# Kernel tuning notes

Measured on AMD Instinct MI355X. Metric: run time of the kernel, lower is better.

## Reference

```python
import jax, jax.numpy as jnp
import numpy as np

B, T, IN, H, NCLS = 128, 512, 4, 256, 3


def _lstm_dir(x_tbi, w_ih, w_hh, b, reverse):
    """One direction of one LSTM layer. x_tbi: [T,B,in] -> ys [T,B,H].
    Gate order matches torch: i, f, g, o."""
    # Precompute input projections for all timesteps (one big GEMM).
    xp = jnp.einsum('tbi,gi->tbg', x_tbi, w_ih) + b  # [T,B,4H]
    nB = x_tbi.shape[1]
    nH = w_hh.shape[1]
    h0 = jnp.zeros((nB, nH), x_tbi.dtype)
    c0 = jnp.zeros((nB, nH), x_tbi.dtype)

    def step(carry, gx):
        h, c = carry
        g = gx + h @ w_hh.T  # [B,4H]
        i, f, gg, o = jnp.split(g, 4, axis=-1)
        c = jax.nn.sigmoid(f) * c + jax.nn.sigmoid(i) * jnp.tanh(gg)
        h = jax.nn.sigmoid(o) * jnp.tanh(c)
        return (h, c), h

    _, ys = jax.lax.scan(step, (h0, c0), xp, reverse=reverse)
    return ys  # [T,B,H], time-aligned with input for both directions


def _bilstm_layer(x_tbi, w_ih, w_hh, b):
    yf = _lstm_dir(x_tbi, w_ih[0], w_hh[0], b[0], reverse=False)
    yb = _lstm_dir(x_tbi, w_ih[1], w_hh[1], b[1], reverse=True)
    return jnp.concatenate([yf, yb], axis=-1)  # [T,B,2H]


def setup_inputs() -> dict:
    key = jax.random.key(0)
    ks = jax.random.split(key, 9)
    s = 0.05
    return {
        'x': jax.random.normal(ks[0], (B, T, IN), jnp.float32),
        'w_ih_l0': jax.random.normal(ks[1], (2, 4 * H, IN), jnp.float32) * s,
        'w_hh_l0': jax.random.normal(ks[2], (2, 4 * H, H), jnp.float32) * s,
        'b_l0': jax.random.normal(ks[3], (2, 4 * H), jnp.float32) * s,
        'w_ih_l1': jax.random.normal(ks[4], (2, 4 * H, 2 * H), jnp.float32) * s,
        'w_hh_l1': jax.random.normal(ks[5], (2, 4 * H, H), jnp.float32) * s,
        'b_l1': jax.random.normal(ks[6], (2, 4 * H), jnp.float32) * s,
        'w_out': jax.random.normal(ks[7], (NCLS, H), jnp.float32) * s,
        'b_out': jax.random.normal(ks[8], (NCLS,), jnp.float32) * s,
    }


def reference(x, w_ih_l0, w_hh_l0, b_l0, w_ih_l1, w_hh_l1, b_l1, w_out, b_out):
    xt = jnp.transpose(x, (1, 0, 2))  # [T,B,4] (time-major for scan)
    b0 = b_l0[:, None, :]  # broadcast over [T,B]
    b1 = b_l1[:, None, :]
    y0 = _bilstm_layer(xt, w_ih_l0, w_hh_l0, b0)   # [T,B,2H]
    y1 = _bilstm_layer(y0, w_ih_l1, w_hh_l1, b1)   # [T,B,2H]
    # sum directions, then take last timestep (torch: out[:,:,:H]+out[:,:,H:], out[:,-1,:])
    last = y1[-1, :, :H] + y1[-1, :, H:]           # [B,H]
    logits = last @ w_out.T + b_out                # [B,3]
    return jax.nn.softmax(logits, axis=1)
```

## Files before the change

### kernel.cpp

```cpp
#include <hip/hip_runtime.h>

typedef __attribute__((ext_vector_type(8))) short bf16x8;
typedef __attribute__((ext_vector_type(4))) float f32x4;
typedef __attribute__((ext_vector_type(4))) int   i32x4;

#define T_LEN 512
#define BATCH 128
#define HID   256
#define G4    1024
#define WPI8_STRIDE 262144

__device__ __forceinline__ float sigmf(float x){
  return __builtin_amdgcn_rcpf(1.0f + __expf(-x));
}
__device__ __forceinline__ float tanhf_(float x){
  return 1.0f - 2.0f*__builtin_amdgcn_rcpf(1.0f + __expf(2.0f*x));
}
__device__ __forceinline__ unsigned short f2bf(float f){
  union{float f;unsigned u;} v; v.f=f;
  unsigned r = v.u + 0x7FFF + ((v.u>>16)&1);
  return (unsigned short)(r>>16);
}
__device__ __forceinline__ float bf2f(unsigned short b){
  union{unsigned u;float f;} v; v.u = ((unsigned)b)<<16; return v.f;
}

__global__ void k_scales(const float* __restrict__ w_hh0, const float* __restrict__ w_hh1,
                         float* __restrict__ comb, float* __restrict__ s_inv){
  int idx = blockIdx.x*256 + threadIdx.x;
  if (idx >= 3*1024) return;
  int dl = idx >> 10, n = idx & 1023;
  const float* src = (dl < 2) ? (w_hh0 + ((size_t)dl*1024 + n)*256)
                              : (w_hh1 + (size_t)n*256);
  float m = 1e-20f;
  for (int k = 0; k < 256; k += 4){
    float4 v = *(const float4*)&src[k];
    m = fmaxf(m, fmaxf(fmaxf(fabsf(v.x), fabsf(v.y)), fmaxf(fabsf(v.z), fabsf(v.w))));
  }
  s_inv[idx] = 127.f / m;
  comb[idx]  = m / 16129.f;
}

__global__ void k_pack_i8(const float* __restrict__ w_hh0, const float* __restrict__ w_hh1,
                          const float* __restrict__ s_inv, char* __restrict__ wp){
  int idx = blockIdx.x*256 + threadIdx.x;
  if (idx >= 3*WPI8_STRIDE) return;
  int j    = idx & 15;
  int lane = (idx >> 4) & 63;
  int kk   = (idx >> 10) & 3;
  int tile = (idx >> 12) & 63;
  int dl   = idx >> 18;
  int g = tile & 3, s = tile >> 2;
  int n = g*256 + s*16 + (lane & 15);
  int k = kk*64 + ((lane >> 4) << 4) + j;
  const float* src = (dl < 2) ? (w_hh0 + ((size_t)dl*1024 + n)*256)
                              : (w_hh1 + (size_t)n*256);
  float v = src[k] * s_inv[dl*1024 + n];
  int q = (int)rintf(fminf(127.f, fmaxf(-127.f, v)));
  wp[idx] = (char)q;
}

__global__ void k_pack_wih1(const float* __restrict__ w, const float* __restrict__ b1,
                            unsigned short* __restrict__ o, float* __restrict__ b1perm){
  int idx = blockIdx.x*256 + threadIdx.x;
  if (idx >= 2*1024*512) return;
  int d     = idx >> 19;
  int rem   = idx & ((1 << 19) - 1);
  int n_out = rem >> 9;
  int k     = rem & 511;
  int n_src = d ? n_out
                : ((n_out & 3)*256 + (n_out >> 6)*16 + ((n_out >> 2) & 15));
  o[idx] = f2bf(w[((size_t)(d*1024 + n_src))*512 + k]);
  if (idx < 1024){
    int ns = (idx & 3)*256 + (idx >> 6)*16 + ((idx >> 2) & 15);
    b1perm[idx] = b1[ns];
  }
}

template<int MODE>
__global__ __launch_bounds__(512, 2) void k_rec4(
    const float* __restrict__ x,
    const char* __restrict__ wpack,
    const float* __restrict__ comb,
    const float* __restrict__ w_ih0,
    const float* __restrict__ b0,
    const unsigned short* __restrict__ xp,
    unsigned short* __restrict__ y0,
    float* __restrict__ hS)
{
  const int tid  = threadIdx.x;
  const int lane = tid & 63;
  const int w    = tid >> 6;
  int dir, bgrp, dl;
  if (MODE == 0){ dir = blockIdx.x >> 5; bgrp = blockIdx.x & 31; dl = dir; }
  else          { dir = 0; bgrp = blockIdx.x; dl = 2; }
  const int b0r = bgrp * 4;

  __shared__ __align__(16) char   A_lds[2][4*288];
  __shared__ __align__(16) float  x_lds[2][4][4];
  __shared__ __align__(16) float4 wv_lds[1024];
  __shared__ float bia_lds[1024];

  const i32x4* wpb = (const i32x4*)(wpack + (size_t)dl*WPI8_STRIDE);
  i32x4 breg[2][4][4];
  #pragma unroll
  for (int p = 0; p < 2; ++p)
    #pragma unroll
    for (int g = 0; g < 4; ++g)
      #pragma unroll
      for (int kk = 0; kk < 4; ++kk)
        breg[p][g][kk] = wpb[(((((2*w+p)*4 + g)*4) + kk) << 6) + lane];

  const int c   = lane & 15;
  const int bl  = lane >> 4;
  const int jc0 = (2*w)*16 + c;
  const int jc1 = jc0 + 16;

  float cmb_l[2][4];
  #pragma unroll
  for (int g = 0; g < 4; ++g){
    cmb_l[0][g] = comb[dl*1024 + g*256 + jc0];
    cmb_l[1][g] = comb[dl*1024 + g*256 + jc1];
  }

  for (int i = tid; i < 2*4*288; i += 512) ((char*)A_lds)[i] = 0;
  if (MODE == 0){
    for (int i = tid; i < 1024; i += 512){
      wv_lds[i]  = *(const float4*)&w_ih0[(size_t)(dir*1024 + i)*4];
      bia_lds[i] = b0[dir*1024 + i];
    }
    if (tid < 16){
      int row = tid >> 2, i = tid & 3;
      int t0 = dir ? (T_LEN-1) : 0;
      x_lds[0][row][i] = x[((size_t)(b0r+row)*T_LEN + t0)*4 + i];
    }
  }

  float c_reg[2] = {0.f, 0.f};

  uint2 cinC[2], cinN[2];
  if (MODE == 1){
    #pragma unroll
    for (int p = 0; p < 2; ++p)
      cinC[p] = *(const uint2*)&xp[((((size_t)0*32 + bgrp)*16 + (2*w+p))*64 + lane)*4];
  }

  for (int tt = 0; tt < T_LEN; ++tt){
    const int t = (MODE == 0 && dir) ? (T_LEN-1-tt) : tt;
    const char* Ac = A_lds[tt & 1];
    char* An = (char*)A_lds[(tt + 1) & 1];

    __syncthreads();

    i32x4 a[4];
    #pragma unroll
    for (int kk = 0; kk < 4; ++kk)
      a[kk] = *(const i32x4*)&Ac[(c >> 2)*288 + kk*64 + ((lane >> 4) << 4)];

    if (MODE == 1){
      int tn = (t + 1 < T_LEN) ? t + 1 : t;
      #pragma unroll
      for (int p = 0; p < 2; ++p)
        cinN[p] = *(const uint2*)&xp[((((size_t)tn*32 + bgrp)*16 + (2*w+p))*64 + lane)*4];
    }

    i32x4 acc[2][4];
    #pragma unroll
    for (int p = 0; p < 2; ++p)
      #pragma unroll
      for (int g = 0; g < 4; ++g){
        acc[p][g] = (i32x4){0,0,0,0};
        #pragma unroll
        for (int kk = 0; kk < 4; ++kk)
          acc[p][g] = __builtin_amdgcn_mfma_i32_16x16x64_i8(a[kk], breg[p][g][kk], acc[p][g], 0, 0, 0);
      }

    float4 xr;
    if (MODE == 0) xr = *(const float4*)&x_lds[tt & 1][bl][0];

    float hv[2];
    #pragma unroll
    for (int p = 0; p < 2; ++p){
      const int jc = p ? jc1 : jc0;
      float gv[4];
      if (MODE == 0){
        #pragma unroll
        for (int g = 0; g < 4; ++g){
          float4 wv4 = wv_lds[g*256 + jc];
          float t0 = fmaf(xr.x, wv4.x, bia_lds[g*256 + jc]);
          t0 = fmaf(xr.y, wv4.y, t0);
          t0 = fmaf(xr.z, wv4.z, t0);
          t0 = fmaf(xr.w, wv4.w, t0);
          gv[g] = fmaf((float)acc[p][g][0], cmb_l[p][g], t0);
        }
      } else {
        unsigned lo = cinC[p].x, hi = cinC[p].y;
        gv[0] = fmaf((float)acc[p][0][0], cmb_l[p][0], bf2f((unsigned short)(lo & 0xFFFF)));
        gv[1] = fmaf((float)acc[p][1][0], cmb_l[p][1], bf2f((unsigned short)(lo >> 16)));
        gv[2] = fmaf((float)acc[p][2][0], cmb_l[p][2], bf2f((unsigned short)(hi & 0xFFFF)));
        gv[3] = fmaf((float)acc[p][3][0], cmb_l[p][3], bf2f((unsigned short)(hi >> 16)));
      }
      float cc = sigmf(gv[1])*c_reg[p] + sigmf(gv[0])*tanhf_(gv[2]);
      c_reg[p] = cc;
      float h = sigmf(gv[3])*tanhf_(cc);
      hv[p] = h;
      float hcl = fminf(127.f, fmaxf(-127.f, h*127.f));
      An[bl*288 + jc] = (char)__float2int_rn(hcl);
      if (MODE == 1 && tt == T_LEN-1)
        hS[(size_t)(b0r + bl)*HID + jc] = h;
    }
    if (MODE == 0){
      unsigned pk;
      asm("v_cvt_pk_bf16_f32 %0, %1, %2" : "=v"(pk) : "v"(hv[0]), "v"(hv[1]));
      size_t yb = ((size_t)t*BATCH + (b0r + bl))*(2*HID) + dir*HID;
      y0[yb + jc0] = (unsigned short)(pk & 0xFFFFu);
      y0[yb + jc1] = (unsigned short)(pk >> 16);
    }

    if (MODE == 0 && tid < 16){
      int tn = dir ? (t > 0 ? t-1 : 0) : (t < T_LEN-1 ? t+1 : t);
      int row = tid >> 2, i = tid & 3;
      x_lds[(tt + 1) & 1][row][i] = x[((size_t)(b0r+row)*T_LEN + tn)*4 + i];
    }
    if (MODE == 1){ cinC[0] = cinN[0]; cinC[1] = cinN[1]; }
  }
}

template<int PLAIN>
__global__ __launch_bounds__(256) void k_gemm_bf(
    const unsigned short* __restrict__ A, const unsigned short* __restrict__ B,
    const float* __restrict__ bias, unsigned short* __restrict__ outF, float* __restrict__ outP)
{
  __shared__ __align__(16) unsigned short As[128*64];
  __shared__ __align__(16) unsigned short Bs[128*64];
  const int tid  = threadIdx.x;
  const int lane = tid & 63;
  const int w = tid >> 6, wm = w >> 1, wn = w & 1;
  const int t  = blockIdx.y;
  const int n0 = blockIdx.x * 128;

  f32x4 acc[4][4];
  #pragma unroll
  for (int i = 0; i < 4; ++i)
    #pragma unroll
    for (int jx = 0; jx < 4; ++jx) acc[i][jx] = (f32x4){0.f,0.f,0.f,0.f};

  const int sr = tid >> 3;
  const int sq = tid & 7;

  for (int k0 = 0; k0 < 512; k0 += 64){
    #pragma unroll
    for (int it = 0; it < 4; ++it){
      int r = sr + it*32;
      uint4 av = *(const uint4*)&A[((size_t)t*128 + r)*512 + k0 + sq*8];
      uint4 bv = *(const uint4*)&B[((size_t)(n0 + r))*512 + k0 + sq*8];
      *(uint4*)&As[r*64 + (sq ^ (r & 7))*8] = av;
      *(uint4*)&Bs[r*64 + (sq ^ (r & 7))*8] = bv;
    }
    __syncthreads();
    bf16x8 af[4][2], bfv[4][2];
    #pragma unroll
    for (int mt = 0; mt < 4; ++mt)
      #pragma unroll
      for (int kk = 0; kk < 2; ++kk){
        int row = wm*64 + mt*16 + (lane & 15);
        af[mt][kk] = *(const bf16x8*)&As[row*64 + ((kk*4 + (lane>>4)) ^ (row & 7))*8];
      }
    #pragma unroll
    for (int nl = 0; nl < 4; ++nl)
      #pragma unroll
      for (int kk = 0; kk < 2; ++kk){
        int row = wn*64 + nl*16 + (lane & 15);
        bfv[nl][kk] = *(const bf16x8*)&Bs[row*64 + ((kk*4 + (lane>>4)) ^ (row & 7))*8];
      }
    #pragma unroll
    for (int mt = 0; mt < 4; ++mt)
      #pragma unroll
      for (int nl = 0; nl < 4; ++nl){
        acc[mt][nl] = __builtin_amdgcn_mfma_f32_16x16x32_bf16(af[mt][0], bfv[nl][0], acc[mt][nl], 0,0,0);
        acc[mt][nl] = __builtin_amdgcn_mfma_f32_16x16x32_bf16(af[mt][1], bfv[nl][1], acc[mt][nl], 0,0,0);
      }
    __syncthreads();
  }

  #pragma unroll
  for (int mt = 0; mt < 4; ++mt){
    #pragma unroll
    for (int nl = 0; nl < 4; ++nl){
      int ng = n0 + wn*64 + nl*16 + (lane & 15);
      float bv = bias[ng];
      f32x4 v = acc[mt][nl];
      if (PLAIN){
        int mrow = wm*64 + mt*16 + (lane >> 4)*4;
        #pragma unroll
        for (int r = 0; r < 4; ++r)
          outP[((size_t)t*128 + mrow + r)*G4 + ng] = v[r] + bv;
      } else {
        int g  = ng & 3;
        int cp = (ng >> 2) & 15;
        int s  = ng >> 6;
        int bbase = wm*64 + mt*16 + ((lane >> 4) << 2);
        int bg = bbase >> 2;
        size_t base = (((size_t)t*32 + bg)*16 + s)*256;
        #pragma unroll
        for (int r = 0; r < 4; ++r)
          outF[base + ((r*16 + cp) << 2) + g] = f2bf(v[r] + bv);
      }
    }
  }
}

__global__ __launch_bounds__(256) void k_final(const float* __restrict__ hS,
                                               const float* __restrict__ xp1b,
                                               const float* __restrict__ w_out,
                                               const float* __restrict__ b_out,
                                               float* __restrict__ out)
{
  const int b = blockIdx.x, j = threadIdx.x;
  float iv = xp1b[b*G4 + 0*HID + j];
  float gv = xp1b[b*G4 + 2*HID + j];
  float ov = xp1b[b*G4 + 3*HID + j];
  float c  = sigmf(iv)*tanhf_(gv);
  float hb = sigmf(ov)*tanhf_(c);
  float last = hS[b*HID + j] + hb;

  __shared__ float part[3][256];
  part[0][j] = last * w_out[0*HID + j];
  part[1][j] = last * w_out[1*HID + j];
  part[2][j] = last * w_out[2*HID + j];
  __syncthreads();
  for (int s = 128; s > 0; s >>= 1){
    if (j < s){
      part[0][j] += part[0][j+s];
      part[1][j] += part[1][j+s];
      part[2][j] += part[2][j+s];
    }
    __syncthreads();
  }
  if (j == 0){
    float l0 = part[0][0] + b_out[0];
    float l1 = part[1][0] + b_out[1];
    float l2 = part[2][0] + b_out[2];
    float m = fmaxf(l0, fmaxf(l1, l2));
    float e0 = __expf(l0-m), e1 = __expf(l1-m), e2 = __expf(l2-m);
    float s = e0 + e1 + e2;
    out[b*3+0] = e0/s; out[b*3+1] = e1/s; out[b*3+2] = e2/s;
  }
}

extern "C" void kernel_launch(void* const* d_in, const int* in_sizes, int n_in,
                              void* d_out, int out_size, void* d_ws, size_t ws_size,
                              hipStream_t stream) {
  const float* x     = (const float*)d_in[0];
  const float* w_ih0 = (const float*)d_in[1];
  const float* w_hh0 = (const float*)d_in[2];
  const float* b0p   = (const float*)d_in[3];
  const float* w_ih1 = (const float*)d_in[4];
  const float* w_hh1 = (const float*)d_in[5];
  const float* b1p   = (const float*)d_in[6];
  const float* w_out = (const float*)d_in[7];
  const float* b_out = (const float*)d_in[8];
  float* out = (float*)d_out;

  unsigned short* y0    = (unsigned short*)d_ws;
  unsigned short* xp1   = y0    + (size_t)T_LEN*BATCH*2*HID;
  unsigned short* wih1p = xp1   + (size_t)T_LEN*BATCH*G4;
  float*          comb  = (float*)(wih1p + 2*G4*2*HID);
  float*          s_inv = comb  + 3*1024;
  float*          b1pm  = s_inv + 3*1024;
  float*          xp1b  = b1pm  + 1024;
  float*          hS    = xp1b  + BATCH*G4;
  char*           wpi8  = (char*)(hS + BATCH*HID);

  k_scales<<<12, 256, 0, stream>>>(w_hh0, w_hh1, comb, s_inv);
  k_pack_i8<<<3072, 256, 0, stream>>>(w_hh0, w_hh1, s_inv, wpi8);
  k_pack_wih1<<<4096, 256, 0, stream>>>(w_ih1, b1p, wih1p, b1pm);

  k_rec4<0><<<64, 512, 0, stream>>>(x, wpi8, comb, w_ih0, b0p, nullptr, y0, nullptr);

  k_gemm_bf<0><<<dim3(8, 512), 256, 0, stream>>>(y0, wih1p, b1pm, xp1, nullptr);

  k_gemm_bf<1><<<dim3(8, 1), 256, 0, stream>>>(y0 + (size_t)(T_LEN-1)*BATCH*2*HID,
                                               wih1p + (size_t)G4*2*HID, b1p + G4,
                                               nullptr, xp1b);

  k_rec4<1><<<32, 512, 0, stream>>>(nullptr, wpi8, comb, nullptr, nullptr, xp1, nullptr, hS);

  k_final<<<BATCH, 256, 0, stream>>>(hS, xp1b, w_out, b_out, out);
}
```

Measured before the change: 1.085 ms.

## Halve batch rows per recurrent block to double block count

The recurrent LSTM kernel now handles 2 batch rows per block instead of 4, so each direction launches twice as many blocks (128 and 64). Each lane now computes one hidden unit instead of two, picking its accumulator element by lane. The layout of the layer-1 input projection written by the GEMM epilogue is changed to match the new per-block packing. This spreads the serial time loop across more CUs and shortens the per-step elementwise work, at the cost of half-empty MFMA tiles and more blocks each loading the full recurrent weights into registers.

```diff
diff --git a/kernel.cpp b/kernel.cpp
--- a/kernel.cpp
+++ b/kernel.cpp
@@ -78,7 +78,7 @@
 }
 
 template<int MODE>
-__global__ __launch_bounds__(512, 2) void k_rec4(
+__global__ __launch_bounds__(512, 2) void k_rec2(
     const float* __restrict__ x,
     const char* __restrict__ wpack,
     const float* __restrict__ comb,
@@ -92,12 +92,12 @@
   const int lane = tid & 63;
   const int w    = tid >> 6;
   int dir, bgrp, dl;
-  if (MODE == 0){ dir = blockIdx.x >> 5; bgrp = blockIdx.x & 31; dl = dir; }
+  if (MODE == 0){ dir = blockIdx.x >> 6; bgrp = blockIdx.x & 63; dl = dir; }
   else          { dir = 0; bgrp = blockIdx.x; dl = 2; }
-  const int b0r = bgrp * 4;
-
-  __shared__ __align__(16) char   A_lds[2][4*288];
-  __shared__ __align__(16) float  x_lds[2][4][4];
+  const int b0r = bgrp * 2;
+
+  __shared__ __align__(16) char   A_lds[2][2*288];
+  __shared__ __align__(16) float  x_lds[2][2][4];
   __shared__ __align__(16) float4 wv_lds[1024];
   __shared__ float bia_lds[1024];
 
@@ -111,39 +111,34 @@
       for (int kk = 0; kk < 4; ++kk)
         breg[p][g][kk] = wpb[(((((2*w+p)*4 + g)*4) + kk) << 6) + lane];
 
-  const int c   = lane & 15;
-  const int bl  = lane >> 4;
-  const int jc0 = (2*w)*16 + c;
-  const int jc1 = jc0 + 16;
-
-  float cmb_l[2][4];
+  const int c  = lane & 15;
+  const int bl = (lane >> 4) & 1;
+  const int pl = lane >> 5;
+  const int jc = (2*w + pl)*16 + c;
+
+  float cmb_l[4];
   #pragma unroll
-  for (int g = 0; g < 4; ++g){
-    cmb_l[0][g] = comb[dl*1024 + g*256 + jc0];
-    cmb_l[1][g] = comb[dl*1024 + g*256 + jc1];
-  }
-
-  for (int i = tid; i < 2*4*288; i += 512) ((char*)A_lds)[i] = 0;
+  for (int g = 0; g < 4; ++g)
+    cmb_l[g] = comb[dl*1024 + g*256 + jc];
+
+  for (int i = tid; i < 2*2*288; i += 512) ((char*)A_lds)[i] = 0;
   if (MODE == 0){
     for (int i = tid; i < 1024; i += 512){
       wv_lds[i]  = *(const float4*)&w_ih0[(size_t)(dir*1024 + i)*4];
       bia_lds[i] = b0[dir*1024 + i];
     }
-    if (tid < 16){
+    if (tid < 8){
       int row = tid >> 2, i = tid & 3;
       int t0 = dir ? (T_LEN-1) : 0;
       x_lds[0][row][i] = x[((size_t)(b0r+row)*T_LEN + t0)*4 + i];
     }
   }
 
-  float c_reg[2] = {0.f, 0.f};
-
-  uint2 cinC[2], cinN[2];
-  if (MODE == 1){
-    #pragma unroll
-    for (int p = 0; p < 2; ++p)
-      cinC[p] = *(const uint2*)&xp[((((size_t)0*32 + bgrp)*16 + (2*w+p))*64 + lane)*4];
-  }
+  float c_reg = 0.f;
+
+  uint2 cinC, cinN;
+  if (MODE == 1)
+    cinC = *(const uint2*)&xp[((((size_t)0*64 + bgrp)*8 + w)*64 + lane)*4];
 
   for (int tt = 0; tt < T_LEN; ++tt){
     const int t = (MODE == 0 && dir) ? (T_LEN-1-tt) : tt;
@@ -155,13 +150,11 @@
     i32x4 a[4];
     #pragma unroll
     for (int kk = 0; kk < 4; ++kk)
-      a[kk] = *(const i32x4*)&Ac[(c >> 2)*288 + kk*64 + ((lane >> 4) << 4)];
+      a[kk] = *(const i32x4*)&Ac[(c & 1)*288 + kk*64 + ((lane >> 4) << 4)];
 
     if (MODE == 1){
       int tn = (t + 1 < T_LEN) ? t + 1 : t;
-      #pragma unroll
-      for (int p = 0; p < 2; ++p)
-        cinN[p] = *(const uint2*)&xp[((((size_t)tn*32 + bgrp)*16 + (2*w+p))*64 + lane)*4];
+      cinN = *(const uint2*)&xp[((((size_t)tn*64 + bgrp)*8 + w)*64 + lane)*4];
     }
 
     i32x4 acc[2][4];
@@ -178,51 +171,45 @@
     float4 xr;
     if (MODE == 0) xr = *(const float4*)&x_lds[tt & 1][bl][0];
 
-    float hv[2];
-    #pragma unroll
-    for (int p = 0; p < 2; ++p){
-      const int jc = p ? jc1 : jc0;
-      float gv[4];
+    float gv[4];
+    #pragma unroll
+    for (int g = 0; g < 4; ++g){
+      int a0 = bl ? acc[0][g][1] : acc[0][g][0];
+      int a1 = bl ? acc[1][g][1] : acc[1][g][0];
+      int ia = pl ? a1 : a0;
       if (MODE == 0){
-        #pragma unroll
-        for (int g = 0; g < 4; ++g){
-          float4 wv4 = wv_lds[g*256 + jc];
-          float t0 = fmaf(xr.x, wv4.x, bia_lds[g*256 + jc]);
-          t0 = fmaf(xr.y, wv4.y, t0);
-          t0 = fmaf(xr.z, wv4.z, t0);
-          t0 = fmaf(xr.w, wv4.w, t0);
-          gv[g] = fmaf((float)acc[p][g][0], cmb_l[p][g], t0);
-        }
+        float4 wv4 = wv_lds[g*256 + jc];
+        float t0 = fmaf(xr.x, wv4.x, bia_lds[g*256 + jc]);
+        t0 = fmaf(xr.y, wv4.y, t0);
+        t0 = fmaf(xr.z, wv4.z, t0);
+        t0 = fmaf(xr.w, wv4.w, t0);
+        gv[g] = fmaf((float)ia, cmb_l[g], t0);
       } else {
-        unsigned lo = cinC[p].x, hi = cinC[p].y;
-        gv[0] = fmaf((float)acc[p][0][0], cmb_l[p][0], bf2f((unsigned short)(lo & 0xFFFF)));
-        gv[1] = fmaf((float)acc[p][1][0], cmb_l[p][1], bf2f((unsigned short)(lo >> 16)));
-        gv[2] = fmaf((float)acc[p][2][0], cmb_l[p][2], bf2f((unsigned short)(hi & 0xFFFF)));
-        gv[3] = fmaf((float)acc[p][3][0], cmb_l[p][3], bf2f((unsigned short)(hi >> 16)));
-      }
-      float cc = sigmf(gv[1])*c_reg[p] + sigmf(gv[0])*tanhf_(gv[2]);
-      c_reg[p] = cc;
-      float h = sigmf(gv[3])*tanhf_(cc);
-      hv[p] = h;
-      float hcl = fminf(127.f, fmaxf(-127.f, h*127.f));
-      An[bl*288 + jc] = (char)__float2int_rn(hcl);
-      if (MODE == 1 && tt == T_LEN-1)
-        hS[(size_t)(b0r + bl)*HID + jc] = h;
-    }
+        unsigned uu = (g < 2) ? cinC.x : cinC.y;
+        float ci = bf2f((unsigned short)((g & 1) ? (uu >> 16) : (uu & 0xFFFF)));
+        gv[g] = fmaf((float)ia, cmb_l[g], ci);
+      }
+    }
+    float cc = sigmf(gv[1])*c_reg + sigmf(gv[0])*tanhf_(gv[2]);
+    c_reg = cc;
+    float h = sigmf(gv[3])*tanhf_(cc);
+    float hcl = fminf(127.f, fmaxf(-127.f, h*127.f));
+    An[bl*288 + jc] = (char)__float2int_rn(hcl);
+
     if (MODE == 0){
       unsigned pk;
-      asm("v_cvt_pk_bf16_f32 %0, %1, %2" : "=v"(pk) : "v"(hv[0]), "v"(hv[1]));
-      size_t yb = ((size_t)t*BATCH + (b0r + bl))*(2*HID) + dir*HID;
-      y0[yb + jc0] = (unsigned short)(pk & 0xFFFFu);
-      y0[yb + jc1] = (unsigned short)(pk >> 16);
-    }
-
-    if (MODE == 0 && tid < 16){
+      asm("v_cvt_pk_bf16_f32 %0, %1, %2" : "=v"(pk) : "v"(h), "v"(h));
+      y0[((size_t)t*BATCH + (b0r + bl))*(2*HID) + dir*HID + jc] = (unsigned short)pk;
+    } else if (tt == T_LEN-1){
+      hS[(size_t)(b0r + bl)*HID + jc] = h;
+    }
+
+    if (MODE == 0 && tid < 8){
       int tn = dir ? (t > 0 ? t-1 : 0) : (t < T_LEN-1 ? t+1 : t);
       int row = tid >> 2, i = tid & 3;
       x_lds[(tt + 1) & 1][row][i] = x[((size_t)(b0r+row)*T_LEN + tn)*4 + i];
     }
-    if (MODE == 1){ cinC[0] = cinN[0]; cinC[1] = cinN[1]; }
+    if (MODE == 1) cinC = cinN;
   }
 }
 
@@ -297,14 +284,16 @@
           outP[((size_t)t*128 + mrow + r)*G4 + ng] = v[r] + bv;
       } else {
         int g  = ng & 3;
-        int cp = (ng >> 2) & 15;
+        int cc = (ng >> 2) & 15;
         int s  = ng >> 6;
-        int bbase = wm*64 + mt*16 + ((lane >> 4) << 2);
-        int bg = bbase >> 2;
-        size_t base = (((size_t)t*32 + bg)*16 + s)*256;
+        int mrow = wm*64 + mt*16 + ((lane >> 4) << 2);
         #pragma unroll
-        for (int r = 0; r < 4; ++r)
-          outF[base + ((r*16 + cp) << 2) + g] = f2bf(v[r] + bv);
+        for (int r = 0; r < 4; ++r){
+          int m  = mrow + r;
+          int bg = m >> 1, bb = m & 1;
+          outF[((((size_t)t*64 + bg)*8 + (s >> 1))*64
+                + (((s & 1) << 5) | (bb << 4) | cc))*4 + g] = f2bf(v[r] + bv);
+        }
       }
     }
   }
@@ -376,7 +365,7 @@
   k_pack_i8<<<3072, 256, 0, stream>>>(w_hh0, w_hh1, s_inv, wpi8);
   k_pack_wih1<<<4096, 256, 0, stream>>>(w_ih1, b1p, wih1p, b1pm);
 
-  k_rec4<0><<<64, 512, 0, stream>>>(x, wpi8, comb, w_ih0, b0p, nullptr, y0, nullptr);
+  k_rec2<0><<<128, 512, 0, stream>>>(x, wpi8, comb, w_ih0, b0p, nullptr, y0, nullptr);
 
   k_gemm_bf<0><<<dim3(8, 512), 256, 0, stream>>>(y0, wih1p, b1pm, xp1, nullptr);
 
@@ -384,7 +373,7 @@
                                                wih1p + (size_t)G4*2*HID, b1p + G4,
                                                nullptr, xp1b);
 
-  k_rec4<1><<<32, 512, 0, stream>>>(nullptr, wpi8, comb, nullptr, nullptr, xp1, nullptr, hS);
+  k_rec2<1><<<64, 512, 0, stream>>>(nullptr, wpi8, comb, nullptr, nullptr, xp1, nullptr, hS);
 
   k_final<<<BATCH, 256, 0, stream>>>(hS, xp1b, w_out, b_out, out);
 }
```

Result: faster. 1.004 ms (-7.5%).
